# Performance work log

Hardware: AMD Instinct MI355X
Metric: run time of the kernel (lower is better)

The kernel has to match this reference:

```python
import jax, jax.numpy as jnp
import numpy as np

N, H, W, C = 4, 128, 128, 128
G = 8
GC = C // G
K = 9  # 3x3 deformable kernel
PAD = 1
HIN, WIN = H + 2 * PAD, W + 2 * PAD
EPS = 1e-5
OFFSET_SCALE = 1.0


def ln(x, g, b):
    m = jnp.mean(x, -1, keepdims=True)
    v = jnp.mean((x - m) ** 2, -1, keepdims=True)
    return (x - m) * jax.lax.rsqrt(v + EPS) * g + b


def gelu(x):
    return jax.nn.gelu(x, approximate=False)


def dcn_core(xp, offset, mask):
    # xp: (N,H,W,C) value features; offset: (N,H,W,G*K*2); mask: (N,H,W,G,K)
    xpad = jnp.pad(xp, ((0, 0), (PAD, PAD), (PAD, PAD), (0, 0)))
    img = xpad.reshape(N, HIN * WIN, G, GC)
    # reference points normalized by padded size (matches dcnv3_core_pytorch)
    ref_x = (jnp.arange(W, dtype=jnp.float32) + 1.5) / WIN  # (dil*(k-1))//2 + 0.5
    ref_y = (jnp.arange(H, dtype=jnp.float32) + 1.5) / HIN
    RX, RY = jnp.meshgrid(ref_x, ref_y)  # (H,W), xy indexing
    ref = jnp.stack([RX, RY], -1)  # (H,W,2) as (x,y)
    gx, gy = jnp.meshgrid(jnp.linspace(-1.0, 1.0, 3), jnp.linspace(-1.0, 1.0, 3), indexing='ij')
    grid = jnp.stack([gx / WIN, gy / HIN], -1).reshape(K, 2)  # dilation grid, x-major
    off = offset.reshape(N, H, W, G, K, 2)
    loc = (ref[None, :, :, None, None, :] + grid * OFFSET_SCALE
           + off * OFFSET_SCALE / jnp.array([WIN, HIN], jnp.float32))  # (N,H,W,G,K,2)
    # grid_sample align_corners=False pixel coords
    px = loc[..., 0] * WIN - 0.5
    py = loc[..., 1] * HIN - 0.5
    x0 = jnp.floor(px); y0 = jnp.floor(py)
    tx = px - x0; ty = py - y0
    x0i = x0.astype(jnp.int32); y0i = y0.astype(jnp.int32)
    x1i = x0i + 1; y1i = y0i + 1

    def gather(iy, ix):
        valid = ((iy >= 0) & (iy < HIN) & (ix >= 0) & (ix < WIN)).astype(xp.dtype)
        idx = jnp.clip(iy, 0, HIN - 1) * WIN + jnp.clip(ix, 0, WIN - 1)  # (N,H,W,G,K)
        idxf = idx.transpose(0, 1, 2, 4, 3).reshape(N, H * W * K, G, 1)
        v = jnp.take_along_axis(img, idxf, axis=1).reshape(N, H, W, K, G, GC)
        return v * valid.transpose(0, 1, 2, 4, 3)[..., None]

    acc = jnp.zeros((N, H, W, G, GC), xp.dtype)
    for iy, ix, wgt in ((y0i, x0i, (1 - ty) * (1 - tx)),
                        (y0i, x1i, (1 - ty) * tx),
                        (y1i, x0i, ty * (1 - tx)),
                        (y1i, x1i, ty * tx)):
        wm = (wgt * mask).transpose(0, 1, 2, 4, 3)[..., None]  # (N,H,W,K,G,1)
        acc = acc + jnp.sum(gather(iy, ix) * wm, axis=3)  # (N,H,W,G,GC)
    return acc.reshape(N, H, W, C)


def dcn(x, in_w, in_b, dw_k, dw_b, dwln_g, dwln_b, off_w, off_b, mask_w, mask_b, out_w, out_b):
    xp = x @ in_w + in_b  # input_proj
    # offset/mask branch: depthwise 3x3 conv on raw input, LN, GELU
    xc = jax.lax.conv_general_dilated(
        x, dw_k.reshape(3, 3, 1, C), (1, 1), 'SAME',
        dimension_numbers=('NHWC', 'HWIO', 'NHWC'), feature_group_count=C) + dw_b
    x1 = gelu(ln(xc, dwln_g, dwln_b))
    offset = x1 @ off_w + off_b  # (N,H,W,G*K*2)
    mask = jax.nn.softmax((x1 @ mask_w + mask_b).reshape(N, H, W, G, K), axis=-1)
    y = dcn_core(xp, offset, mask)
    return y @ out_w + out_b


def _forward(x, ln1_g, ln1_b, in_w, in_b, dw_k, dw_b, dwln_g, dwln_b, off_w, off_b,
             mask_w, mask_b, out_w, out_b, ln2_g, ln2_b, fc1_w, fc1_b, fc2_w, fc2_b):
    # pre-norm, no layer_scale, no drop_path (rate 0)
    x = x + dcn(ln(x, ln1_g, ln1_b), in_w, in_b, dw_k, dw_b, dwln_g, dwln_b,
                off_w, off_b, mask_w, mask_b, out_w, out_b)
    h = ln(x, ln2_g, ln2_b)
    h = gelu(h @ fc1_w + fc1_b) @ fc2_w + fc2_b
    return x + h


def setup_inputs() -> dict:
    key = jax.random.key(0)
    ks = jax.random.split(key, 10)

    def lin(k, fin, fout, scale=1.0):
        s = scale / np.sqrt(fin)
        return jax.random.uniform(k, (fin, fout), minval=-s, maxval=s, dtype=jnp.float32)

    d = {}
    d['x'] = jax.random.normal(ks[0], (N, H, W, C), dtype=jnp.float32)
    d['ln1_g'] = jnp.ones((C,), jnp.float32); d['ln1_b'] = jnp.zeros((C,), jnp.float32)
    d['in_w'] = lin(ks[1], C, C); d['in_b'] = jnp.zeros((C,), jnp.float32)
    d['dw_k'] = jax.random.normal(ks[2], (3, 3, C), dtype=jnp.float32) * 0.05
    d['dw_b'] = jnp.zeros((C,), jnp.float32)
    d['dwln_g'] = jnp.ones((C,), jnp.float32); d['dwln_b'] = jnp.zeros((C,), jnp.float32)
    d['off_w'] = lin(ks[3], C, G * K * 2, 0.1); d['off_b'] = jnp.zeros((G * K * 2,), jnp.float32)
    d['mask_w'] = lin(ks[4], C, G * K, 0.1); d['mask_b'] = jnp.zeros((G * K,), jnp.float32)
    d['out_w'] = lin(ks[5], C, C); d['out_b'] = jnp.zeros((C,), jnp.float32)
    d['ln2_g'] = jnp.ones((C,), jnp.float32); d['ln2_b'] = jnp.zeros((C,), jnp.float32)
    d['fc1_w'] = lin(ks[6], C, 4 * C); d['fc1_b'] = jnp.zeros((4 * C,), jnp.float32)
    d['fc2_w'] = lin(ks[7], 4 * C, C); d['fc2_b'] = jnp.zeros((C,), jnp.float32)
    return d


def reference(x, ln1_g, ln1_b, in_w, in_b, dw_k, dw_b, dwln_g, dwln_b, off_w, off_b,
              mask_w, mask_b, out_w, out_b, ln2_g, ln2_b, fc1_w, fc1_b, fc2_w, fc2_b):
    return _forward(x, ln1_g, ln1_b, in_w, in_b, dw_k, dw_b, dwln_g, dwln_b, off_w, off_b,
                    mask_w, mask_b, out_w, out_b, ln2_g, ln2_b, fc1_w, fc1_b, fc2_w, fc2_b)
```

## Files before the change

### kernel.cpp

```cpp
#include <hip/hip_runtime.h>
#include <hip/hip_bf16.h>
#include <math.h>

#define NB 4
#define HH 128
#define WW 128
#define CC 128
#define GG 8
#define GCC 16
#define KK 9
#define NHW (NB*HH*WW)

typedef __hip_bfloat16 bf16;
typedef __attribute__((ext_vector_type(8))) short short8;
typedef __attribute__((ext_vector_type(4))) float f32x4;

__device__ __forceinline__ float b2f(bf16 v){ return __bfloat162float(v); }
__device__ __forceinline__ bf16 f2b(float v){ return __float2bfloat16(v); }
__device__ __forceinline__ float gelu_f(float v){
  float x = fabsf(v) * 0.70710678118654752f;
  float t = __builtin_amdgcn_rcpf(fmaf(0.3275911f, x, 1.0f));
  float p = t*fmaf(t, fmaf(t, fmaf(t, fmaf(t, 1.061405429f, -1.453152027f),
                         1.421413741f), -0.284496736f), 0.254829592f);
  float e = __expf(-x*x);
  float er = copysignf(fmaf(-p, e, 1.0f), v);
  return 0.5f*v*(1.0f+er);
}
__device__ __forceinline__ float lo_bf(unsigned u){ union{unsigned i; float f;} c; c.i = u<<16; return c.f; }
__device__ __forceinline__ float hi_bf(unsigned u){ union{unsigned i; float f;} c; c.i = u&0xffff0000u; return c.f; }
__device__ __forceinline__ unsigned pk(float a, float b){
  return ((unsigned)__bfloat16_as_ushort(f2b(b))<<16) | (unsigned)__bfloat16_as_ushort(f2b(a));
}
__device__ __forceinline__ void st_out(bf16* p, float v){ *p = f2b(v); }
__device__ __forceinline__ void st_out(float* p, float v){ *p = v; }
__device__ __forceinline__ void acc8(float* a, uint4 u, float w){
  a[0]+=w*lo_bf(u.x); a[1]+=w*hi_bf(u.x); a[2]+=w*lo_bf(u.y); a[3]+=w*hi_bf(u.y);
  a[4]+=w*lo_bf(u.z); a[5]+=w*hi_bf(u.z); a[6]+=w*lo_bf(u.w); a[7]+=w*hi_bf(u.w);
}

__global__ __launch_bounds__(256) void prep_k(
    const float* __restrict__ inw,  const float* __restrict__ outw,
    const float* __restrict__ fc1w, const float* __restrict__ fc2w,
    const float* __restrict__ offw, const float* __restrict__ offb,
    const float* __restrict__ maskw,const float* __restrict__ maskb,
    bf16* __restrict__ inwt, bf16* __restrict__ outwt,
    bf16* __restrict__ w1t,  bf16* __restrict__ w2t,
    bf16* __restrict__ wsw,  float* __restrict__ cw)
{
  int idx = blockIdx.x*256 + threadIdx.x;
  if (idx < 16384){
    int n = idx>>7, k = idx&127;
    inwt[idx] = f2b(inw[(size_t)k*128 + n]);
  } else if (idx < 32768){
    int i = idx-16384; int n = i>>7, k = i&127;
    outwt[i] = f2b(outw[(size_t)k*128 + n]);
  } else if (idx < 98304){
    int i = idx-32768; int n = i>>7, k = i&127;
    w1t[i] = f2b(fc1w[(size_t)k*512 + n]);
  } else if (idx < 163840){
    int i = idx-98304; int n = i>>9, k = i&511;
    w2t[i] = f2b(fc2w[(size_t)k*128 + n]);
  } else if (idx < 192512){
    int i = idx-163840; int nn = i>>7, k = i&127;
    float v = (nn<144) ? offw[(size_t)k*144+nn] : (nn<216 ? maskw[(size_t)k*72+(nn-144)] : 0.f);
    wsw[i] = f2b(v);
  } else if (idx < 192736){
    int i = idx-192512;
    cw[i] = (i<144) ? offb[i] : (i<216 ? maskb[i-144] : 0.f);
  }
}

__global__ __launch_bounds__(256) void ln_k(const float* __restrict__ X,
    const float* __restrict__ gam, const float* __restrict__ bet, bf16* __restrict__ Y)
{
  int lane = threadIdx.x & 63;
  int wid  = threadIdx.x >> 6;
  size_t pix = (size_t)blockIdx.x*4 + wid;
  const float* xp = X + pix*CC;
  int c0 = lane*2;
  float v0 = xp[c0], v1 = xp[c0+1];
  float s = v0+v1, ss = v0*v0+v1*v1;
  #pragma unroll
  for (int off=32; off>0; off>>=1){ s += __shfl_xor(s,off,64); ss += __shfl_xor(ss,off,64); }
  float mean = s*(1.f/CC);
  float var  = ss*(1.f/CC) - mean*mean;
  float rstd = rsqrtf(var + 1e-5f);
  float y0 = (v0-mean)*rstd*gam[c0]   + bet[c0];
  float y1 = (v1-mean)*rstd*gam[c0+1] + bet[c0+1];
  Y[pix*CC + c0]   = f2b(y0);
  Y[pix*CC + c0+1] = f2b(y1);
}

__global__ __launch_bounds__(256) void convln_k(const bf16* __restrict__ XN,
    const float* __restrict__ dwk, const float* __restrict__ dwb,
    const float* __restrict__ gam, const float* __restrict__ bet, bf16* __restrict__ X1)
{
  int tid = threadIdx.x;
  int px = tid>>4, cg = tid&15;
  int ch0 = cg*8;
  int pix = blockIdx.x*16 + px;
  int w = pix & (WW-1), h = (pix>>7)&(HH-1), n = pix>>14;
  float acc[8];
  {
    float4 b0 = *(const float4*)(dwb + ch0), b1 = *(const float4*)(dwb + ch0 + 4);
    acc[0]=b0.x; acc[1]=b0.y; acc[2]=b0.z; acc[3]=b0.w;
    acc[4]=b1.x; acc[5]=b1.y; acc[6]=b1.z; acc[7]=b1.w;
  }
  #pragma unroll
  for (int ky=0;ky<3;ky++){
    int yy = h+ky-1; if ((unsigned)yy>=(unsigned)HH) continue;
    #pragma unroll
    for (int kx=0;kx<3;kx++){
      int xx = w+kx-1; if ((unsigned)xx>=(unsigned)WW) continue;
      uint4 u = *(const uint4*)(XN + ((size_t)((n*HH+yy)*WW+xx))*CC + ch0);
      const float* wp = dwk + (ky*3+kx)*CC + ch0;
      float4 w0 = *(const float4*)wp; float4 w1 = *(const float4*)(wp+4);
      acc[0] += lo_bf(u.x)*w0.x; acc[1] += hi_bf(u.x)*w0.y;
      acc[2] += lo_bf(u.y)*w0.z; acc[3] += hi_bf(u.y)*w0.w;
      acc[4] += lo_bf(u.z)*w1.x; acc[5] += hi_bf(u.z)*w1.y;
      acc[6] += lo_bf(u.w)*w1.z; acc[7] += hi_bf(u.w)*w1.w;
    }
  }
  float s=0.f, ss=0.f;
  #pragma unroll
  for (int i=0;i<8;i++){ s += acc[i]; ss += acc[i]*acc[i]; }
  #pragma unroll
  for (int off=1; off<16; off<<=1){ s += __shfl_xor(s,off,64); ss += __shfl_xor(ss,off,64); }
  float mean=s*(1.f/CC), var=ss*(1.f/CC)-mean*mean, rstd=rsqrtf(var+1e-5f);
  float4 g0 = *(const float4*)(gam + ch0), g1 = *(const float4*)(gam + ch0 + 4);
  float4 be0 = *(const float4*)(bet + ch0), be1 = *(const float4*)(bet + ch0 + 4);
  float gv[8] = {g0.x,g0.y,g0.z,g0.w,g1.x,g1.y,g1.z,g1.w};
  float bv[8] = {be0.x,be0.y,be0.z,be0.w,be1.x,be1.y,be1.z,be1.w};
  float o[8];
  #pragma unroll
  for (int i=0;i<8;i++) o[i] = gelu_f((acc[i]-mean)*rstd*gv[i] + bv[i]);
  uint4 up; up.x = pk(o[0],o[1]); up.y = pk(o[2],o[3]); up.z = pk(o[4],o[5]); up.w = pk(o[6],o[7]);
  *(uint4*)(X1 + (size_t)pix*CC + ch0) = up;
}

#define OMS 226
__global__ __launch_bounds__(256) void samp_k(const bf16* __restrict__ X1,
    const bf16* __restrict__ XP,
    const bf16* __restrict__ wsw, const float* __restrict__ cw,
    bf16* __restrict__ Y)
{
  __shared__ bf16 oms[32*OMS];
  int tid = threadIdx.x;
  int pix0 = blockIdx.x*32;
  int wave = tid>>6, l = tid&63, lo16 = l&15, quad = l>>4;
  int nt0 = wave*4;
  int ntn = (wave==3) ? 2 : 4;
  short8 af[2][4];
  #pragma unroll
  for (int mt=0;mt<2;mt++)
    #pragma unroll
    for (int ks=0;ks<4;ks++)
      af[mt][ks] = *(const short8*)(X1 + (size_t)(pix0+mt*16+lo16)*128 + ks*32 + quad*8);
  f32x4 z = {0.f,0.f,0.f,0.f};
  f32x4 acc[2][4];
  #pragma unroll
  for (int mt=0;mt<2;mt++)
    #pragma unroll
    for (int t=0;t<4;t++) acc[mt][t]=z;
  for (int t=0;t<ntn;t++){
    int nt = nt0+t;
    #pragma unroll
    for (int ks=0;ks<4;ks++){
      short8 bfr = *(const short8*)(wsw + (size_t)(nt*16+lo16)*128 + ks*32 + quad*8);
      acc[0][t] = __builtin_amdgcn_mfma_f32_16x16x32_bf16(af[0][ks], bfr, acc[0][t], 0,0,0);
      acc[1][t] = __builtin_amdgcn_mfma_f32_16x16x32_bf16(af[1][ks], bfr, acc[1][t], 0,0,0);
    }
  }
  for (int t=0;t<ntn;t++){
    int col = (nt0+t)*16 + lo16;
    float bb = cw[col];
    #pragma unroll
    for (int mt=0;mt<2;mt++)
      #pragma unroll
      for (int r=0;r<4;r++)
        oms[(mt*16 + quad*4 + r)*OMS + col] = f2b(acc[mt][t][r] + bb);
  }
  __syncthreads();
  {
    int m = tid>>3, g = tid&7;
    int base = m*OMS + 144 + g*9;
    float sc[9]; float mx = -1e30f;
    #pragma unroll
    for (int k=0;k<9;k++){ sc[k] = b2f(oms[base+k]); mx = fmaxf(mx, sc[k]); }
    float sum = 0.f;
    #pragma unroll
    for (int k=0;k<9;k++){ sc[k] = expf(sc[k]-mx); sum += sc[k]; }
    float inv = 1.f/sum;
    #pragma unroll
    for (int k=0;k<9;k++) oms[base+k] = f2b(sc[k]*inv);
  }
  __syncthreads();
  int oct = tid&15, sl = tid>>4;
  int g = oct>>1;
  int ch = g*GCC + (oct&1)*8;
  int w0 = pix0 & (WW-1);
  int h  = (pix0>>7) & (HH-1);
  int n  = pix0>>14;
  const bf16* base = XP + (size_t)n*HH*WW*CC + ch;
  for (int it=0; it<2; it++){
    int m = it*16 + sl;
    int wc = w0 + m;
    const bf16* omrow = &oms[m*OMS];
    float a[8] = {0.f,0.f,0.f,0.f,0.f,0.f,0.f,0.f};
    #pragma unroll
    for (int k=0;k<9;k++){
      float offx = b2f(omrow[g*18 + 2*k]);
      float offy = b2f(omrow[g*18 + 2*k + 1]);
      float mk   = b2f(omrow[144 + g*9 + k]);
      float pxf = (float)(wc + (k/3) - 1) + offx;
      float pyf = (float)(h  + (k%3) - 1) + offy;
      float x0f = floorf(pxf), y0f = floorf(pyf);
      float txf = pxf-x0f,     tyf = pyf-y0f;
      int x0 = (int)x0f, y0 = (int)y0f;
      int x1i = x0+1,    y1i = y0+1;
      float vx0 = ((unsigned)x0 <(unsigned)WW)?1.f:0.f;
      float vx1 = ((unsigned)x1i<(unsigned)WW)?1.f:0.f;
      float vy0 = ((unsigned)y0 <(unsigned)HH)?1.f:0.f;
      float vy1 = ((unsigned)y1i<(unsigned)HH)?1.f:0.f;
      int cx0 = min(max(x0,0),WW-1),  cx1 = min(max(x1i,0),WW-1);
      int cy0 = min(max(y0,0),HH-1),  cy1 = min(max(y1i,0),HH-1);
      float w00=(1.f-tyf)*(1.f-txf)*mk*vy0*vx0, w01=(1.f-tyf)*txf*mk*vy0*vx1;
      float w10=tyf*(1.f-txf)*mk*vy1*vx0,       w11=tyf*txf*mk*vy1*vx1;
      uint4 u00 = *(const uint4*)(base + ((size_t)(cy0*WW+cx0))*CC);
      uint4 u01 = *(const uint4*)(base + ((size_t)(cy0*WW+cx1))*CC);
      uint4 u10 = *(const uint4*)(base + ((size_t)(cy1*WW+cx0))*CC);
      uint4 u11 = *(const uint4*)(base + ((size_t)(cy1*WW+cx1))*CC);
      acc8(a,u00,w00); acc8(a,u01,w01); acc8(a,u10,w10); acc8(a,u11,w11);
    }
    uint4 outp;
    outp.x = pk(a[0],a[1]); outp.y = pk(a[2],a[3]);
    outp.z = pk(a[4],a[5]); outp.w = pk(a[6],a[7]);
    *(uint4*)(Y + (size_t)(pix0+m)*CC + ch) = outp;
  }
}

template<typename OutT, bool RES>
__global__ __launch_bounds__(256) void gemm_mfma(const bf16* __restrict__ A,
    const bf16* __restrict__ Bt, const float* __restrict__ bias,
    const float* __restrict__ res, OutT* __restrict__ C)
{
  int tid = threadIdx.x;
  int wave = tid>>6, l = tid&63, lo16 = l&15, quad = l>>4;
  int m0 = blockIdx.y*256 + wave*64;
  int n0 = blockIdx.x*64;
  short8 bfr[4][4];
  #pragma unroll
  for (int ks=0;ks<4;ks++)
    #pragma unroll
    for (int nt=0;nt<4;nt++)
      bfr[ks][nt] = *(const short8*)(Bt + (size_t)(n0+nt*16+lo16)*128 + ks*32 + quad*8);
  f32x4 z = {0.f,0.f,0.f,0.f};
  f32x4 acc[4][4];
  #pragma unroll
  for (int mt=0;mt<4;mt++)
    #pragma unroll
    for (int nt=0;nt<4;nt++) acc[mt][nt]=z;
  #pragma unroll
  for (int ks=0;ks<4;ks++){
    short8 af[4];
    #pragma unroll
    for (int mt=0;mt<4;mt++)
      af[mt] = *(const short8*)(A + (size_t)(m0+mt*16+lo16)*128 + ks*32 + quad*8);
    #pragma unroll
    for (int nt=0;nt<4;nt++)
      #pragma unroll
      for (int mt=0;mt<4;mt++)
        acc[mt][nt] = __builtin_amdgcn_mfma_f32_16x16x32_bf16(af[mt], bfr[ks][nt], acc[mt][nt], 0,0,0);
  }
  #pragma unroll
  for (int mt=0;mt<4;mt++)
    #pragma unroll
    for (int nt=0;nt<4;nt++){
      int col = n0 + nt*16 + lo16;
      float bb = bias[col];
      #pragma unroll
      for (int r=0;r<4;r++){
        int row = m0 + mt*16 + quad*4 + r;
        float v = acc[mt][nt][r] + bb;
        if (RES) v += res[(size_t)row*128 + col];
        st_out(&C[(size_t)row*128 + col], v);
      }
    }
}

__global__ __launch_bounds__(256) void mlp_mfma(const float* __restrict__ X2,
    const float* __restrict__ lng, const float* __restrict__ lnb,
    const bf16* __restrict__ w1t, const float* __restrict__ b1,
    const bf16* __restrict__ w2t, const float* __restrict__ b2,
    float* __restrict__ OUT)
{
  __shared__ __align__(16) char smem[53248];
  bf16* h0s = (bf16*)smem;
  bf16* ts  = (bf16*)smem;
  bf16* w1s = (bf16*)(smem + 17408);
  bf16* w2s = (bf16*)(smem + 34816);
  int tid = threadIdx.x;
  int wave = tid>>6, l = tid&63, lo16 = l&15, quad = l>>4;
  int m0 = blockIdx.x*128;
  int t8 = tid*8;
  #pragma unroll
  for (int itn=0; itn<2; itn++){
    int px = (tid>>2) + itn*64;
    int q = tid&3;
    const float* xr = X2 + (size_t)(m0+px)*128 + q*32;
    float v[32];
    #pragma unroll
    for (int i=0;i<8;i++) *(float4*)(v+i*4) = *(const float4*)(xr+i*4);
    float s=0.f, ss=0.f;
    #pragma unroll
    for (int i=0;i<32;i++){ s += v[i]; ss += v[i]*v[i]; }
    s  += __shfl_xor(s,1,64);  ss += __shfl_xor(ss,1,64);
    s  += __shfl_xor(s,2,64);  ss += __shfl_xor(ss,2,64);
    float mean = s*(1.f/CC), var = ss*(1.f/CC)-mean*mean, rstd = rsqrtf(var+1e-5f);
    const float* gp = lng + q*32; const float* bp = lnb + q*32;
    uint4* dst = (uint4*)(&h0s[px*136 + q*32]);
    #pragma unroll
    for (int i=0;i<4;i++){
      float4 g0 = *(const float4*)(gp+i*8),  g1 = *(const float4*)(gp+i*8+4);
      float4 c0v = *(const float4*)(bp+i*8), c1v = *(const float4*)(bp+i*8+4);
      float o0 = (v[i*8+0]-mean)*rstd*g0.x + c0v.x;
      float o1 = (v[i*8+1]-mean)*rstd*g0.y + c0v.y;
      float o2 = (v[i*8+2]-mean)*rstd*g0.z + c0v.z;
      float o3 = (v[i*8+3]-mean)*rstd*g0.w + c0v.w;
      float o4 = (v[i*8+4]-mean)*rstd*g1.x + c1v.x;
      float o5 = (v[i*8+5]-mean)*rstd*g1.y + c1v.y;
      float o6 = (v[i*8+6]-mean)*rstd*g1.z + c1v.z;
      float o7 = (v[i*8+7]-mean)*rstd*g1.w + c1v.w;
      uint4 up; up.x = pk(o0,o1); up.y = pk(o2,o3); up.z = pk(o4,o5); up.w = pk(o6,o7);
      dst[i] = up;
    }
  }
  __syncthreads();
  short8 a1[2][4];
  #pragma unroll
  for (int mt=0;mt<2;mt++)
    #pragma unroll
    for (int ks=0;ks<4;ks++)
      a1[mt][ks] = *(const short8*)(&h0s[(wave*32 + mt*16 + lo16)*136 + ks*32 + quad*8]);
  f32x4 z = {0.f,0.f,0.f,0.f};
  f32x4 acc2[2][8];
  #pragma unroll
  for (int mt=0;mt<2;mt++)
    #pragma unroll
    for (int nt=0;nt<8;nt++) acc2[mt][nt]=z;

  for (int c0=0;c0<512;c0+=64){
    __syncthreads();
    #pragma unroll
    for (int it=0;it<4;it++){
      int e = it*2048 + t8;
      *(uint4*)(&w1s[(e>>7)*136 + (e&127)]) =
          *(const uint4*)(w1t + (size_t)(c0 + (e>>7))*128 + (e&127));
      *(uint4*)(&w2s[(e>>6)*72 + (e&63)]) =
          *(const uint4*)(w2t + (size_t)(e>>6)*512 + c0 + (e&63));
    }
    __syncthreads();
    f32x4 acc1[2][4];
    #pragma unroll
    for (int mt=0;mt<2;mt++)
      #pragma unroll
      for (int nt=0;nt<4;nt++) acc1[mt][nt]=z;
    #pragma unroll
    for (int ks=0;ks<4;ks++)
      #pragma unroll
      for (int nt=0;nt<4;nt++){
        short8 bfr = *(const short8*)(&w1s[(nt*16+lo16)*136 + ks*32 + quad*8]);
        acc1[0][nt] = __builtin_amdgcn_mfma_f32_16x16x32_bf16(a1[0][ks], bfr, acc1[0][nt], 0,0,0);
        acc1[1][nt] = __builtin_amdgcn_mfma_f32_16x16x32_bf16(a1[1][ks], bfr, acc1[1][nt], 0,0,0);
      }
    #pragma unroll
    for (int mt=0;mt<2;mt++)
      #pragma unroll
      for (int nt=0;nt<4;nt++){
        float bb = b1[c0 + nt*16 + lo16];
        #pragma unroll
        for (int r=0;r<4;r++)
          ts[(wave*32 + mt*16 + quad*4 + r)*68 + nt*16 + lo16] = f2b(gelu_f(acc1[mt][nt][r] + bb));
      }
    __syncthreads();
    #pragma unroll
    for (int ks2=0;ks2<2;ks2++){
      short8 a2[2];
      #pragma unroll
      for (int mt=0;mt<2;mt++)
        a2[mt] = *(const short8*)(&ts[(wave*32 + mt*16 + lo16)*68 + ks2*32 + quad*8]);
      #pragma unroll
      for (int nt2=0;nt2<8;nt2++){
        short8 bfr2 = *(const short8*)(&w2s[(nt2*16+lo16)*72 + ks2*32 + quad*8]);
        acc2[0][nt2] = __builtin_amdgcn_mfma_f32_16x16x32_bf16(a2[0], bfr2, acc2[0][nt2], 0,0,0);
        acc2[1][nt2] = __builtin_amdgcn_mfma_f32_16x16x32_bf16(a2[1], bfr2, acc2[1][nt2], 0,0,0);
      }
    }
  }
  #pragma unroll
  for (int mt=0;mt<2;mt++)
    #pragma unroll
    for (int nt=0;nt<8;nt++){
      int col = nt*16 + lo16;
      float bb = b2[col];
      #pragma unroll
      for (int r=0;r<4;r++){
        int row = m0 + wave*32 + mt*16 + quad*4 + r;
        float v = acc2[mt][nt][r] + bb + X2[(size_t)row*128 + col];
        OUT[(size_t)row*128 + col] = v;
      }
    }
}

extern "C" void kernel_launch(void* const* d_in, const int* in_sizes, int n_in,
                              void* d_out, int out_size, void* d_ws, size_t ws_size,
                              hipStream_t stream)
{
  const float* x    = (const float*)d_in[0];
  const float* ln1g = (const float*)d_in[1];
  const float* ln1b = (const float*)d_in[2];
  const float* inw  = (const float*)d_in[3];
  const float* inb  = (const float*)d_in[4];
  const float* dwk  = (const float*)d_in[5];
  const float* dwb  = (const float*)d_in[6];
  const float* dwlng= (const float*)d_in[7];
  const float* dwlnb= (const float*)d_in[8];
  const float* offw = (const float*)d_in[9];
  const float* offb = (const float*)d_in[10];
  const float* maskw= (const float*)d_in[11];
  const float* maskb= (const float*)d_in[12];
  const float* outw = (const float*)d_in[13];
  const float* outb = (const float*)d_in[14];
  const float* ln2g = (const float*)d_in[15];
  const float* ln2b = (const float*)d_in[16];
  const float* fc1w = (const float*)d_in[17];
  const float* fc1b = (const float*)d_in[18];
  const float* fc2w = (const float*)d_in[19];
  const float* fc2b = (const float*)d_in[20];
  float* out = (float*)d_out;

  bf16* ws = (bf16*)d_ws;
  const size_t S = (size_t)NHW*CC;
  bf16* xn = ws;
  bf16* xp = ws + S;
  bf16* x1 = ws + 2*S;
  bf16* y  = xn;
  float* x2 = out;
  bf16* inwt  = ws + 3*S;
  bf16* outwt = inwt + 128*128;
  bf16* w1t   = outwt + 128*128;
  bf16* w2t   = w1t + 512*128;
  bf16* wsw   = w2t + 128*512;
  float* cw   = (float*)(wsw + 224*128);

  prep_k<<<753, 256, 0, stream>>>(inw, outw, fc1w, fc2w, offw, offb, maskw, maskb,
                                  inwt, outwt, w1t, w2t, wsw, cw);
  ln_k<<<NHW/4, 256, 0, stream>>>(x, ln1g, ln1b, xn);
  gemm_mfma<bf16,false><<<dim3(2,256), 256, 0, stream>>>(xn, inwt, inb, nullptr, xp);
  convln_k<<<NHW/16, 256, 0, stream>>>(xn, dwk, dwb, dwlng, dwlnb, x1);
  samp_k<<<NHW/32, 256, 0, stream>>>(x1, xp, wsw, cw, y);
  gemm_mfma<float,true><<<dim3(2,256), 256, 0, stream>>>(y, outwt, outb, x, x2);
  mlp_mfma<<<NHW/128, 256, 0, stream>>>(x2, ln2g, ln2b, w1t, fc1b, w2t, fc2b, out);
}
```

Baseline: 292.3 us.

## Read MLP weights directly from global memory and drop block-wide barriers

```diff
diff --git a/kernel.cpp b/kernel.cpp
--- a/kernel.cpp
+++ b/kernel.cpp
@@ -294,33 +294,28 @@
     const bf16* __restrict__ w2t, const float* __restrict__ b2,
     float* __restrict__ OUT)
 {
-  __shared__ __align__(16) char smem[53248];
+  __shared__ __align__(16) char smem[34816 + 17408];
   bf16* h0s = (bf16*)smem;
-  bf16* ts  = (bf16*)smem;
-  bf16* w1s = (bf16*)(smem + 17408);
-  bf16* w2s = (bf16*)(smem + 34816);
+  bf16* ts  = (bf16*)(smem + 34816);
   int tid = threadIdx.x;
   int wave = tid>>6, l = tid&63, lo16 = l&15, quad = l>>4;
   int m0 = blockIdx.x*128;
-  int t8 = tid*8;
-  #pragma unroll
-  for (int itn=0; itn<2; itn++){
-    int px = (tid>>2) + itn*64;
-    int q = tid&3;
-    const float* xr = X2 + (size_t)(m0+px)*128 + q*32;
-    float v[32];
-    #pragma unroll
-    for (int i=0;i<8;i++) *(float4*)(v+i*4) = *(const float4*)(xr+i*4);
+  {
+    int row = wave*32 + (l>>1);
+    int half = l&1;
+    const float* xr = X2 + (size_t)(m0+row)*128 + half*64;
+    float v[64];
+    #pragma unroll
+    for (int i=0;i<16;i++) *(float4*)(v+i*4) = *(const float4*)(xr+i*4);
     float s=0.f, ss=0.f;
     #pragma unroll
-    for (int i=0;i<32;i++){ s += v[i]; ss += v[i]*v[i]; }
+    for (int i=0;i<64;i++){ s += v[i]; ss += v[i]*v[i]; }
     s  += __shfl_xor(s,1,64);  ss += __shfl_xor(ss,1,64);
-    s  += __shfl_xor(s,2,64);  ss += __shfl_xor(ss,2,64);
     float mean = s*(1.f/CC), var = ss*(1.f/CC)-mean*mean, rstd = rsqrtf(var+1e-5f);
-    const float* gp = lng + q*32; const float* bp = lnb + q*32;
-    uint4* dst = (uint4*)(&h0s[px*136 + q*32]);
-    #pragma unroll
-    for (int i=0;i<4;i++){
+    const float* gp = lng + half*64; const float* bp = lnb + half*64;
+    uint4* dst = (uint4*)(&h0s[row*136 + half*64]);
+    #pragma unroll
+    for (int i=0;i<8;i++){
       float4 g0 = *(const float4*)(gp+i*8),  g1 = *(const float4*)(gp+i*8+4);
       float4 c0v = *(const float4*)(bp+i*8), c1v = *(const float4*)(bp+i*8+4);
       float o0 = (v[i*8+0]-mean)*rstd*g0.x + c0v.x;
@@ -335,7 +330,6 @@
       dst[i] = up;
     }
   }
-  __syncthreads();
   short8 a1[2][4];
   #pragma unroll
   for (int mt=0;mt<2;mt++)
@@ -350,16 +344,6 @@
     for (int nt=0;nt<8;nt++) acc2[mt][nt]=z;
 
   for (int c0=0;c0<512;c0+=64){
-    __syncthreads();
-    #pragma unroll
-    for (int it=0;it<4;it++){
-      int e = it*2048 + t8;
-      *(uint4*)(&w1s[(e>>7)*136 + (e&127)]) =
-          *(const uint4*)(w1t + (size_t)(c0 + (e>>7))*128 + (e&127));
-      *(uint4*)(&w2s[(e>>6)*72 + (e&63)]) =
-          *(const uint4*)(w2t + (size_t)(e>>6)*512 + c0 + (e&63));
-    }
-    __syncthreads();
     f32x4 acc1[2][4];
     #pragma unroll
     for (int mt=0;mt<2;mt++)
@@ -369,7 +353,7 @@
     for (int ks=0;ks<4;ks++)
       #pragma unroll
       for (int nt=0;nt<4;nt++){
-        short8 bfr = *(const short8*)(&w1s[(nt*16+lo16)*136 + ks*32 + quad*8]);
+        short8 bfr = *(const short8*)(w1t + (size_t)(c0 + nt*16+lo16)*128 + ks*32 + quad*8);
         acc1[0][nt] = __builtin_amdgcn_mfma_f32_16x16x32_bf16(a1[0][ks], bfr, acc1[0][nt], 0,0,0);
         acc1[1][nt] = __builtin_amdgcn_mfma_f32_16x16x32_bf16(a1[1][ks], bfr, acc1[1][nt], 0,0,0);
       }
@@ -382,7 +366,6 @@
         for (int r=0;r<4;r++)
           ts[(wave*32 + mt*16 + quad*4 + r)*68 + nt*16 + lo16] = f2b(gelu_f(acc1[mt][nt][r] + bb));
       }
-    __syncthreads();
     #pragma unroll
     for (int ks2=0;ks2<2;ks2++){
       short8 a2[2];
@@ -391,7 +374,7 @@
         a2[mt] = *(const short8*)(&ts[(wave*32 + mt*16 + lo16)*68 + ks2*32 + quad*8]);
       #pragma unroll
       for (int nt2=0;nt2<8;nt2++){
-        short8 bfr2 = *(const short8*)(&w2s[(nt2*16+lo16)*72 + ks2*32 + quad*8]);
+        short8 bfr2 = *(const short8*)(w2t + (size_t)(nt2*16+lo16)*512 + c0 + ks2*32 + quad*8);
         acc2[0][nt2] = __builtin_amdgcn_mfma_f32_16x16x32_bf16(a2[0], bfr2, acc2[0][nt2], 0,0,0);
         acc2[1][nt2] = __builtin_amdgcn_mfma_f32_16x16x32_bf16(a2[1], bfr2, acc2[1][nt2], 0,0,0);
       }
```

Result: slower. 312.5 us (+6.9%).

## Compute MLP LayerNorm directly into MFMA fragments and share one weight buffer

Applied to the files above, without the earlier changes.

```diff
diff --git a/kernel.cpp b/kernel.cpp
--- a/kernel.cpp
+++ b/kernel.cpp
@@ -294,54 +294,49 @@
     const bf16* __restrict__ w2t, const float* __restrict__ b2,
     float* __restrict__ OUT)
 {
-  __shared__ __align__(16) char smem[53248];
-  bf16* h0s = (bf16*)smem;
-  bf16* ts  = (bf16*)smem;
-  bf16* w1s = (bf16*)(smem + 17408);
-  bf16* w2s = (bf16*)(smem + 34816);
+  __shared__ __align__(16) char smem[18432 + 17408];
+  bf16* wsm = (bf16*)smem;
+  bf16* ts  = (bf16*)(smem + 18432);
   int tid = threadIdx.x;
   int wave = tid>>6, l = tid&63, lo16 = l&15, quad = l>>4;
   int m0 = blockIdx.x*128;
   int t8 = tid*8;
-  #pragma unroll
-  for (int itn=0; itn<2; itn++){
-    int px = (tid>>2) + itn*64;
-    int q = tid&3;
-    const float* xr = X2 + (size_t)(m0+px)*128 + q*32;
-    float v[32];
-    #pragma unroll
-    for (int i=0;i<8;i++) *(float4*)(v+i*4) = *(const float4*)(xr+i*4);
-    float s=0.f, ss=0.f;
-    #pragma unroll
-    for (int i=0;i<32;i++){ s += v[i]; ss += v[i]*v[i]; }
-    s  += __shfl_xor(s,1,64);  ss += __shfl_xor(ss,1,64);
-    s  += __shfl_xor(s,2,64);  ss += __shfl_xor(ss,2,64);
-    float mean = s*(1.f/CC), var = ss*(1.f/CC)-mean*mean, rstd = rsqrtf(var+1e-5f);
-    const float* gp = lng + q*32; const float* bp = lnb + q*32;
-    uint4* dst = (uint4*)(&h0s[px*136 + q*32]);
-    #pragma unroll
-    for (int i=0;i<4;i++){
-      float4 g0 = *(const float4*)(gp+i*8),  g1 = *(const float4*)(gp+i*8+4);
-      float4 c0v = *(const float4*)(bp+i*8), c1v = *(const float4*)(bp+i*8+4);
-      float o0 = (v[i*8+0]-mean)*rstd*g0.x + c0v.x;
-      float o1 = (v[i*8+1]-mean)*rstd*g0.y + c0v.y;
-      float o2 = (v[i*8+2]-mean)*rstd*g0.z + c0v.z;
-      float o3 = (v[i*8+3]-mean)*rstd*g0.w + c0v.w;
-      float o4 = (v[i*8+4]-mean)*rstd*g1.x + c1v.x;
-      float o5 = (v[i*8+5]-mean)*rstd*g1.y + c1v.y;
-      float o6 = (v[i*8+6]-mean)*rstd*g1.z + c1v.z;
-      float o7 = (v[i*8+7]-mean)*rstd*g1.w + c1v.w;
-      uint4 up; up.x = pk(o0,o1); up.y = pk(o2,o3); up.z = pk(o4,o5); up.w = pk(o6,o7);
-      dst[i] = up;
-    }
-  }
-  __syncthreads();
   short8 a1[2][4];
-  #pragma unroll
-  for (int mt=0;mt<2;mt++)
-    #pragma unroll
-    for (int ks=0;ks<4;ks++)
-      a1[mt][ks] = *(const short8*)(&h0s[(wave*32 + mt*16 + lo16)*136 + ks*32 + quad*8]);
+  {
+    float gv[32], bv[32];
+    #pragma unroll
+    for (int ks=0;ks<4;ks++){
+      *(float4*)(gv+ks*8)   = *(const float4*)(lng + ks*32 + quad*8);
+      *(float4*)(gv+ks*8+4) = *(const float4*)(lng + ks*32 + quad*8 + 4);
+      *(float4*)(bv+ks*8)   = *(const float4*)(lnb + ks*32 + quad*8);
+      *(float4*)(bv+ks*8+4) = *(const float4*)(lnb + ks*32 + quad*8 + 4);
+    }
+    #pragma unroll
+    for (int mt=0;mt<2;mt++){
+      int row = m0 + wave*32 + mt*16 + lo16;
+      const float* xr = X2 + (size_t)row*128;
+      float v[32];
+      #pragma unroll
+      for (int ks=0;ks<4;ks++){
+        *(float4*)(v+ks*8)   = *(const float4*)(xr + ks*32 + quad*8);
+        *(float4*)(v+ks*8+4) = *(const float4*)(xr + ks*32 + quad*8 + 4);
+      }
+      float s=0.f, ss=0.f;
+      #pragma unroll
+      for (int i=0;i<32;i++){ s += v[i]; ss += v[i]*v[i]; }
+      s += __shfl_xor(s,16,64); ss += __shfl_xor(ss,16,64);
+      s += __shfl_xor(s,32,64); ss += __shfl_xor(ss,32,64);
+      float mean = s*(1.f/CC), var = ss*(1.f/CC)-mean*mean, rstd = rsqrtf(var+1e-5f);
+      #pragma unroll
+      for (int ks=0;ks<4;ks++){
+        short8 t;
+        #pragma unroll
+        for (int j=0;j<8;j++)
+          t[j] = (short)__bfloat16_as_ushort(f2b((v[ks*8+j]-mean)*rstd*gv[ks*8+j] + bv[ks*8+j]));
+        a1[mt][ks] = t;
+      }
+    }
+  }
   f32x4 z = {0.f,0.f,0.f,0.f};
   f32x4 acc2[2][8];
   #pragma unroll
@@ -354,10 +349,8 @@
     #pragma unroll
     for (int it=0;it<4;it++){
       int e = it*2048 + t8;
-      *(uint4*)(&w1s[(e>>7)*136 + (e&127)]) =
+      *(uint4*)(&wsm[(e>>7)*136 + (e&127)]) =
           *(const uint4*)(w1t + (size_t)(c0 + (e>>7))*128 + (e&127));
-      *(uint4*)(&w2s[(e>>6)*72 + (e&63)]) =
-          *(const uint4*)(w2t + (size_t)(e>>6)*512 + c0 + (e&63));
     }
     __syncthreads();
     f32x4 acc1[2][4];
@@ -369,7 +362,7 @@
     for (int ks=0;ks<4;ks++)
       #pragma unroll
       for (int nt=0;nt<4;nt++){
-        short8 bfr = *(const short8*)(&w1s[(nt*16+lo16)*136 + ks*32 + quad*8]);
+        short8 bfr = *(const short8*)(&wsm[(nt*16+lo16)*136 + ks*32 + quad*8]);
         acc1[0][nt] = __builtin_amdgcn_mfma_f32_16x16x32_bf16(a1[0][ks], bfr, acc1[0][nt], 0,0,0);
         acc1[1][nt] = __builtin_amdgcn_mfma_f32_16x16x32_bf16(a1[1][ks], bfr, acc1[1][nt], 0,0,0);
       }
@@ -384,6 +377,13 @@
       }
     __syncthreads();
     #pragma unroll
+    for (int it=0;it<4;it++){
+      int e = it*2048 + t8;
+      *(uint4*)(&wsm[(e>>6)*72 + (e&63)]) =
+          *(const uint4*)(w2t + (size_t)(e>>6)*512 + c0 + (e&63));
+    }
+    __syncthreads();
+    #pragma unroll
     for (int ks2=0;ks2<2;ks2++){
       short8 a2[2];
       #pragma unroll
@@ -391,7 +391,7 @@
         a2[mt] = *(const short8*)(&ts[(wave*32 + mt*16 + lo16)*68 + ks2*32 + quad*8]);
       #pragma unroll
       for (int nt2=0;nt2<8;nt2++){
-        short8 bfr2 = *(const short8*)(&w2s[(nt2*16+lo16)*72 + ks2*32 + quad*8]);
+        short8 bfr2 = *(const short8*)(&wsm[(nt2*16+lo16)*72 + ks2*32 + quad*8]);
         acc2[0][nt2] = __builtin_amdgcn_mfma_f32_16x16x32_bf16(a2[0], bfr2, acc2[0][nt2], 0,0,0);
         acc2[1][nt2] = __builtin_amdgcn_mfma_f32_16x16x32_bf16(a2[1], bfr2, acc2[1][nt2], 0,0,0);
       }
```

Result: no change. 290.3 us (-0.7%).
